# Kernel tuning notes

Hardware: AMD Instinct MI355X
Metric: run time of the kernel (lower is better)

The kernel has to match this reference:

```python
import jax, jax.numpy as jnp
import numpy as np

B, S, D, H = 2, 2048, 1024, 16
DH = D // H  # 64


def setup_inputs() -> dict:
    key = jax.random.key(0)
    k1, k2, k3, k4 = jax.random.split(key, 4)
    x = jax.random.normal(k1, (B, S, D), dtype=jnp.float32)
    # causal mask: 0 => masked (matches mask==0 -> -inf in source)
    mask = jnp.tril(jnp.ones((S, S), dtype=jnp.int32))
    Wq = jax.random.normal(k2, (H, D, DH), dtype=jnp.float32) * (D ** -0.5)
    Wk = jax.random.normal(k3, (H, D, DH), dtype=jnp.float32) * (D ** -0.5)
    Wo = jax.random.normal(k4, (D, D), dtype=jnp.float32) * (D ** -0.5)
    bo = jnp.zeros((D,), dtype=jnp.float32)
    return {"x": x, "mask": mask, "Wq": Wq, "Wk": Wk, "Wo": Wo, "bo": bo}


def reference(x, mask, Wq, Wk, Wo, bo):
    # Per source: q = query(x), k = key(x), v = query(x)  (bug kept: v == q)
    q = jnp.einsum('bsd,hde->bhse', x, Wq)   # [B,H,S,DH]
    k = jnp.einsum('bsd,hde->bhse', x, Wk)   # [B,H,S,DH]
    # scale uses d_model (input dim), not d_head -- faithful to source
    scale = jnp.asarray(D, x.dtype) ** -0.5
    scores = jnp.einsum('bhse,bhte->bhst', q, k) * scale  # [B,H,S,S]
    neg_inf = jnp.asarray(float('-inf'), scores.dtype)
    scores = jnp.where(mask[None, None, :, :] == 0, neg_inf, scores)
    w = jax.nn.softmax(scores, axis=-1)
    attn = jnp.einsum('bhst,bhte->bhse', w, q)  # v == q
    # concat heads: head axis becomes contiguous feature blocks
    attn = attn.transpose(0, 2, 1, 3).reshape(B, S, D)
    return attn @ Wo + bo
```

## Files before the change

kernel.cpp:

```cpp
#include <hip/hip_runtime.h>
#include <hip/hip_bf16.h>

#define BQ 2
#define SQ 2048
#define DMODEL 1024
#define NH 16
#define DH 64
#define NQT (SQ / 64)

typedef __attribute__((ext_vector_type(8))) short bf16x8;
typedef __attribute__((ext_vector_type(4))) short bf16x4;
typedef __attribute__((ext_vector_type(4))) float f32x4;
typedef unsigned short u16;

__device__ __forceinline__ u16 f2b(float f) {
  __hip_bfloat16 h = __float2bfloat16(f);
  return *reinterpret_cast<u16*>(&h);
}

__device__ __forceinline__ unsigned packbf(float lo, float hi) {
  return ((unsigned)f2b(hi) << 16) | (unsigned)f2b(lo);
}

#define MFMA(a, b, c) __builtin_amdgcn_mfma_f32_16x16x32_bf16((a), (b), (c), 0, 0, 0)

__device__ __forceinline__ f32x4 mfma16(bf16x4 a, bf16x4 b, f32x4 c) {
  asm("v_mfma_f32_16x16x16_bf16 %0, %1, %2, %0" : "+v"(c) : "v"(a), "v"(b));
  return c;
}

__device__ __forceinline__ unsigned cvtpk(float lo, float hi) {
  unsigned r;
  asm("v_cvt_pk_bf16_f32 %0, %1, %2" : "=v"(r) : "v"(lo), "v"(hi));
  return r;
}

#define CS (0.03125f * 1.44269504088896f)

__global__ __launch_bounds__(256) void prep_kernel(
    const float* __restrict__ Wq, const float* __restrict__ Wk,
    const float* __restrict__ Wo, const float* __restrict__ x,
    u16* __restrict__ WqT, u16* __restrict__ WkT, u16* __restrict__ WoT,
    u16* __restrict__ xb) {
  __shared__ alignas(16) u16 T[64][72];
  int xt = blockIdx.x, yt = blockIdx.y, z = blockIdx.z;
  int tid = threadIdx.x;
  if (z == 3) {
    int idx = (yt * 16 + xt) * 256 + tid;
    const int nchunks = BQ * SQ * DMODEL / 4;
    for (int i = idx; i < nchunks; i += 65536) {
      float4 v = *(const float4*)&x[(size_t)i * 4];
      uint2 o;
      o.x = packbf(v.x, v.y);
      o.y = packbf(v.z, v.w);
      *(uint2*)&xb[(size_t)i * 4] = o;
    }
    return;
  }
  if (z < 2) {
    const float* W = z ? Wk : Wq;
    u16* WT = z ? WkT : WqT;
    const float* src = W + ((size_t)yt * 1024 + xt * 64) * 64;
#pragma unroll
    for (int i = 0; i < 4; ++i) {
      int lin = tid + i * 256;
      int r = lin >> 4, c4 = (lin & 15) * 4;
      float4 v = *(const float4*)&src[(size_t)r * 64 + c4];
      *(unsigned*)&T[r][c4]     = packbf(v.x, v.y);
      *(unsigned*)&T[r][c4 + 2] = packbf(v.z, v.w);
    }
    __syncthreads();
#pragma unroll
    for (int i = 0; i < 2; ++i) {
      int lin = tid + i * 256;
      int e = lin >> 3, d8 = (lin & 7) * 8;
      u16 tmp[8];
#pragma unroll
      for (int j = 0; j < 8; ++j) tmp[j] = T[d8 + j][e];
      *(uint4*)&WT[((size_t)yt * 64 + e) * 1024 + xt * 64 + d8] = *(uint4*)tmp;
    }
  } else {
    const float* src = Wo + ((size_t)xt * 64) * 1024 + yt * 64;
#pragma unroll
    for (int i = 0; i < 4; ++i) {
      int lin = tid + i * 256;
      int r = lin >> 4, c4 = (lin & 15) * 4;
      float4 v = *(const float4*)&src[(size_t)r * 1024 + c4];
      *(unsigned*)&T[r][c4]     = packbf(v.x, v.y);
      *(unsigned*)&T[r][c4 + 2] = packbf(v.z, v.w);
    }
    __syncthreads();
#pragma unroll
    for (int i = 0; i < 2; ++i) {
      int lin = tid + i * 256;
      int n = lin >> 3, k8 = (lin & 7) * 8;
      u16 tmp[8];
#pragma unroll
      for (int j = 0; j < 8; ++j) tmp[j] = T[k8 + j][n];
      *(uint4*)&WoT[((size_t)yt * 64 + n) * 1024 + xt * 64 + k8] = *(uint4*)tmp;
    }
  }
}

__global__ __launch_bounds__(256) void transpose_q_kernel(
    const u16* __restrict__ Q, u16* __restrict__ QT) {
  __shared__ alignas(16) u16 T[64][72];
  int st = blockIdx.x, h = blockIdx.y, b = blockIdx.z;
  size_t hb = ((size_t)(b * NH + h)) * SQ * DH;
  int tid = threadIdx.x;
#pragma unroll
  for (int i2 = 0; i2 < 2; ++i2) {
    int c = tid + i2 * 256;
    int r = c >> 3, cc = (c & 7) * 8;
    *(uint4*)&T[r][cc] = *(const uint4*)&Q[hb + (size_t)(st * 64 + r) * DH + cc];
  }
  __syncthreads();
#pragma unroll
  for (int i2 = 0; i2 < 2; ++i2) {
    int c = tid + i2 * 256;
    int e = c >> 3, s8 = (c & 7) * 8;
    u16 tmp[8];
#pragma unroll
    for (int j = 0; j < 8; ++j) tmp[j] = T[s8 + j][e];
    *(uint4*)&QT[hb + (size_t)e * SQ + st * 64 + s8] = *(uint4*)tmp;
  }
}


__global__ __launch_bounds__(256) void proj_kernel(
    const u16* __restrict__ xb,
    const u16* __restrict__ Wcat,
    u16* __restrict__ Qb, u16* __restrict__ Kb,
    u16* __restrict__ QT) {
  __shared__ alignas(16) u16 Xs[64][72];
  __shared__ alignas(16) u16 Ws[64][72];
  int st = blockIdx.x, hy = blockIdx.y, b = blockIdx.z;
  int tid = threadIdx.x, w = tid >> 6, l = tid & 63;
  int lr = l & 15, hi = l >> 4, lk = hi * 8;
  int r0s = tid >> 3, cc0 = (tid & 7) * 8, r1s = r0s + 32;
  f32x4 acc[4] = {};
  const u16* Ab = xb + (size_t)(b * SQ + st * 64) * DMODEL;
  const u16* Wb = Wcat + (size_t)hy * DH * DMODEL;

  *(uint4*)&Xs[r0s][cc0] = *(const uint4*)&Ab[(size_t)r0s * DMODEL + cc0];
  *(uint4*)&Xs[r1s][cc0] = *(const uint4*)&Ab[(size_t)r1s * DMODEL + cc0];
  *(uint4*)&Ws[r0s][cc0] = *(const uint4*)&Wb[(size_t)r0s * DMODEL + cc0];
  *(uint4*)&Ws[r1s][cc0] = *(const uint4*)&Wb[(size_t)r1s * DMODEL + cc0];
  __syncthreads();

  uint4 xr0 = *(const uint4*)&Ab[(size_t)r0s * DMODEL + 64 + cc0];
  uint4 xr1 = *(const uint4*)&Ab[(size_t)r1s * DMODEL + 64 + cc0];
  uint4 wv0 = *(const uint4*)&Wb[(size_t)r0s * DMODEL + 64 + cc0];
  uint4 wv1 = *(const uint4*)&Wb[(size_t)r1s * DMODEL + 64 + cc0];

  for (int ks = 0; ks < 16; ++ks) {
#pragma unroll
    for (int kk = 0; kk < 2; ++kk) {
      bf16x8 a = *(const bf16x8*)&Xs[w * 16 + lr][kk * 32 + lk];
#pragma unroll
      for (int n = 0; n < 4; ++n) {
        bf16x8 bb = *(const bf16x8*)&Ws[n * 16 + lr][kk * 32 + lk];
        acc[n] = MFMA(a, bb, acc[n]);
      }
    }
    if (ks < 15) {
      __syncthreads();
      *(uint4*)&Xs[r0s][cc0] = xr0;
      *(uint4*)&Xs[r1s][cc0] = xr1;
      *(uint4*)&Ws[r0s][cc0] = wv0;
      *(uint4*)&Ws[r1s][cc0] = wv1;
      if (ks + 2 < 16) {
        int k0 = (ks + 2) * 64;
        xr0 = *(const uint4*)&Ab[(size_t)r0s * DMODEL + k0 + cc0];
        xr1 = *(const uint4*)&Ab[(size_t)r1s * DMODEL + k0 + cc0];
        wv0 = *(const uint4*)&Wb[(size_t)r0s * DMODEL + k0 + cc0];
        wv1 = *(const uint4*)&Wb[(size_t)r1s * DMODEL + k0 + cc0];
      }
      __syncthreads();
    }
  }

  bool isQ = (hy < NH);
  float scale = isQ ? 1.0f : CS;
  int hh = hy & (NH - 1);
  size_t hbh = ((size_t)(b * NH + hh)) * SQ * DH;
  size_t obase = hbh + (size_t)st * 64 * DH;
  int r0 = w * 16 + (hi << 2);
  u16 (*Cs)[72] = Xs;
  __syncthreads();
#pragma unroll
  for (int n = 0; n < 4; ++n)
#pragma unroll
    for (int r = 0; r < 4; ++r)
      Cs[r0 + r][n * 16 + lr] = f2b(acc[n][r] * scale);
  __syncthreads();

  u16* dst = isQ ? Qb : Kb;
#pragma unroll
  for (int i2 = 0; i2 < 2; ++i2) {
    int lin = tid + i2 * 256;
    int r = lin >> 3, c8 = (lin & 7) * 8;
    *(uint4*)&dst[obase + (size_t)r * DH + c8] = *(const uint4*)&Cs[r][c8];
  }
  if (isQ && QT) {
#pragma unroll
    for (int i2 = 0; i2 < 2; ++i2) {
      int lin = tid + i2 * 256;
      int e = lin >> 3, s8 = (lin & 7) * 8;
      u16 tmp[8];
#pragma unroll
      for (int j = 0; j < 8; ++j) tmp[j] = Cs[s8 + j][e];
      *(uint4*)&QT[hbh + (size_t)e * SQ + st * 64 + s8] = *(uint4*)tmp;
    }
  }
}


__global__ __launch_bounds__(512) void attn_kernel(
    const u16* __restrict__ Qt,
    const u16* __restrict__ Kt,
    const u16* __restrict__ QTt,
    u16* __restrict__ Oc) {
  __shared__ alignas(16) u16 Ks[2][64][72];
  __shared__ alignas(16) u16 Vs[2][64][72];
  int bx = blockIdx.x, h = blockIdx.y, b = blockIdx.z;
  int p = b ? bx : (15 - bx);
  int tid = threadIdx.x, w = tid >> 6, l = tid & 63;
  int lr = l & 15, hi = l >> 4, lk = hi * 8;
  int qtile = 2 * p + (w >> 2);
  int q0 = qtile * 64 + (w & 3) * 16;
  int jmax = 2 * p + 1;
  size_t hb = ((size_t)(b * NH + h)) * SQ * DH;

  int r0s = tid >> 3, cc0 = (tid & 7) * 8;

  bf16x8 aq[2];
  {
    const u16* qrow = Qt + hb + (size_t)(q0 + lr) * DH;
    aq[0] = *(const bf16x8*)&qrow[lk];
    aq[1] = *(const bf16x8*)&qrow[32 + lk];
  }

  *(uint4*)&Ks[0][r0s][cc0] = *(const uint4*)&Kt[hb + (size_t)r0s * DH + cc0];
  *(uint4*)&Vs[0][r0s][cc0] = *(const uint4*)&QTt[hb + (size_t)r0s * SQ + cc0];
  __syncthreads();

  uint4 kreg = *(const uint4*)&Kt[hb + (size_t)(64 + r0s) * DH + cc0];
  uint4 vreg = *(const uint4*)&QTt[hb + (size_t)r0s * SQ + 64 + cc0];

  f32x4 acc_t[4] = {};
  float l_run = 0.f;
  int cur = 0;

  for (int j = 0; j <= jmax; ++j) {
    if (j <= qtile) {
      f32x4 s[4] = {};
#pragma unroll
      for (int kk = 0; kk < 2; ++kk)
#pragma unroll
        for (int n = 0; n < 4; ++n) {
          bf16x8 bk = *(const bf16x8*)&Ks[cur][n * 16 + lr][kk * 32 + lk];
          s[n] = MFMA(bk, aq[kk], s[n]);
        }

      if (j == qtile) {
        int qg = q0 + lr;
#pragma unroll
        for (int n = 0; n < 4; ++n) {
          int kbase = j * 64 + n * 16 + hi * 4;
#pragma unroll
          for (int r = 0; r < 4; ++r)
            s[n][r] = (kbase + r > qg) ? 0.f : exp2f(s[n][r]);
        }
      } else {
#pragma unroll
        for (int n = 0; n < 4; ++n)
#pragma unroll
          for (int r = 0; r < 4; ++r) s[n][r] = exp2f(s[n][r]);
      }

#pragma unroll
      for (int n = 0; n < 4; ++n)
        l_run += (s[n][0] + s[n][1]) + (s[n][2] + s[n][3]);

      bf16x4 pb[4];
#pragma unroll
      for (int n = 0; n < 4; ++n) {
        uint2 u;
        u.x = cvtpk(s[n][0], s[n][1]);
        u.y = cvtpk(s[n][2], s[n][3]);
        pb[n] = *(bf16x4*)&u;
      }

#pragma unroll
      for (int nv = 0; nv < 4; ++nv) {
        const u16* vrow = &Vs[cur][nv * 16 + lr][hi * 4];
#pragma unroll
        for (int nh = 0; nh < 4; ++nh) {
          bf16x4 va = *(const bf16x4*)&vrow[nh * 16];
          acc_t[nv] = mfma16(va, pb[nh], acc_t[nv]);
        }
      }
    }

    if (j < jmax) {
      *(uint4*)&Ks[cur ^ 1][r0s][cc0] = kreg;
      *(uint4*)&Vs[cur ^ 1][r0s][cc0] = vreg;
      if (j + 2 <= jmax) {
        kreg = *(const uint4*)&Kt[hb + (size_t)((j + 2) * 64 + r0s) * DH + cc0];
        vreg = *(const uint4*)&QTt[hb + (size_t)r0s * SQ + (j + 2) * 64 + cc0];
      }
      __syncthreads();
      cur ^= 1;
    }
  }

  l_run += __shfl_xor(l_run, 16, 64);
  l_run += __shfl_xor(l_run, 32, 64);
  float inv = 1.f / l_run;

  size_t rbase = ((size_t)b * SQ + q0 + lr) * DMODEL + h * DH;
#pragma unroll
  for (int nv = 0; nv < 4; ++nv) {
    uint2 pw;
    pw.x = cvtpk(acc_t[nv][0] * inv, acc_t[nv][1] * inv);
    pw.y = cvtpk(acc_t[nv][2] * inv, acc_t[nv][3] * inv);
    *(uint2*)&Oc[rbase + nv * 16 + hi * 4] = pw;
  }
}


__global__ __launch_bounds__(256) void outproj_kernel(
    const u16* __restrict__ Oc,
    const u16* __restrict__ WoT,
    const float* __restrict__ bo,
    float* __restrict__ out) {
  __shared__ alignas(16) u16 Xs[64][72];
  __shared__ alignas(16) u16 Ws[64][72];
  int rt = blockIdx.x, nt = blockIdx.y;
  int tid = threadIdx.x, w = tid >> 6, l = tid & 63;
  int lr = l & 15, lk = (l >> 4) * 8;
  int r0s = tid >> 3, cc0 = (tid & 7) * 8, r1s = r0s + 32;
  f32x4 acc[4] = {};
  const u16* Ab = Oc + (size_t)rt * 64 * DMODEL;
  const u16* Wb = WoT + (size_t)nt * 64 * DMODEL;

  *(uint4*)&Xs[r0s][cc0] = *(const uint4*)&Ab[(size_t)r0s * DMODEL + cc0];
  *(uint4*)&Xs[r1s][cc0] = *(const uint4*)&Ab[(size_t)r1s * DMODEL + cc0];
  *(uint4*)&Ws[r0s][cc0] = *(const uint4*)&Wb[(size_t)r0s * DMODEL + cc0];
  *(uint4*)&Ws[r1s][cc0] = *(const uint4*)&Wb[(size_t)r1s * DMODEL + cc0];
  __syncthreads();

  uint4 xr0 = *(const uint4*)&Ab[(size_t)r0s * DMODEL + 64 + cc0];
  uint4 xr1 = *(const uint4*)&Ab[(size_t)r1s * DMODEL + 64 + cc0];
  uint4 wv0 = *(const uint4*)&Wb[(size_t)r0s * DMODEL + 64 + cc0];
  uint4 wv1 = *(const uint4*)&Wb[(size_t)r1s * DMODEL + 64 + cc0];

  for (int ks = 0; ks < 16; ++ks) {
#pragma unroll
    for (int kk = 0; kk < 2; ++kk) {
      bf16x8 a = *(const bf16x8*)&Xs[w * 16 + lr][kk * 32 + lk];
#pragma unroll
      for (int n = 0; n < 4; ++n) {
        bf16x8 bb = *(const bf16x8*)&Ws[n * 16 + lr][kk * 32 + lk];
        acc[n] = MFMA(a, bb, acc[n]);
      }
    }
    if (ks < 15) {
      __syncthreads();
      *(uint4*)&Xs[r0s][cc0] = xr0;
      *(uint4*)&Xs[r1s][cc0] = xr1;
      *(uint4*)&Ws[r0s][cc0] = wv0;
      *(uint4*)&Ws[r1s][cc0] = wv1;
      if (ks + 2 < 16) {
        int k0 = (ks + 2) * 64;
        xr0 = *(const uint4*)&Ab[(size_t)r0s * DMODEL + k0 + cc0];
        xr1 = *(const uint4*)&Ab[(size_t)r1s * DMODEL + k0 + cc0];
        wv0 = *(const uint4*)&Wb[(size_t)r0s * DMODEL + k0 + cc0];
        wv1 = *(const uint4*)&Wb[(size_t)r1s * DMODEL + k0 + cc0];
      }
      __syncthreads();
    }
  }

  int r0 = w * 16 + ((l >> 4) << 2);
#pragma unroll
  for (int n = 0; n < 4; ++n) {
    int col = nt * 64 + n * 16 + lr;
    float bv = bo[col];
#pragma unroll
    for (int r = 0; r < 4; ++r)
      out[(size_t)(rt * 64 + r0 + r) * DMODEL + col] = acc[n][r] + bv;
  }
}


extern "C" void kernel_launch(void* const* d_in, const int* in_sizes, int n_in,
                              void* d_out, int out_size, void* d_ws, size_t ws_size,
                              hipStream_t stream) {
  const float* x  = (const float*)d_in[0];
  const float* Wq = (const float*)d_in[2];
  const float* Wk = (const float*)d_in[3];
  const float* Wo = (const float*)d_in[4];
  const float* bo = (const float*)d_in[5];
  float* out = (float*)d_out;

  char* ws = (char*)d_ws;
  u16* xb  = (u16*)ws;
  u16* WqT = xb + (size_t)BQ * SQ * DMODEL;
  u16* WkT = WqT + (size_t)NH * DH * DMODEL;
  u16* WoT = WkT + (size_t)NH * DH * DMODEL;
  u16* Qb  = WoT + (size_t)DMODEL * DMODEL;
  u16* Kb  = Qb + (size_t)BQ * NH * SQ * DH;
  u16* Ob  = Kb + (size_t)BQ * NH * SQ * DH;
  u16* QTnew = Ob + (size_t)BQ * SQ * DMODEL;

  size_t need = ((size_t)QTnew - (size_t)ws) + (size_t)BQ * SQ * DMODEL * sizeof(u16);
  bool fused = ws_size >= need;
  u16* QTb = fused ? QTnew : xb;

  prep_kernel<<<dim3(16, 16, 4), 256, 0, stream>>>(Wq, Wk, Wo, x, WqT, WkT, WoT, xb);

  proj_kernel<<<dim3(SQ / 64, 2 * NH, BQ), 256, 0, stream>>>(
      xb, WqT, Qb, Kb, fused ? QTb : (u16*)nullptr);
  if (!fused)
    transpose_q_kernel<<<dim3(SQ / 64, NH, BQ), 256, 0, stream>>>(Qb, QTb);
  attn_kernel<<<dim3(16, NH, BQ), 512, 0, stream>>>(Qb, Kb, QTb, Ob);
  outproj_kernel<<<dim3(BQ * SQ / 64, DMODEL / 64, 1), 256, 0, stream>>>(Ob, WoT, bo, out);
}
```

Baseline: 107.3 us.

## Split KV range across two wave groups per query tile and reduce partials

The attention kernel previously gave each block a pair of query tiles (paired for causal load balance), with both 4-wave groups sharing a serial double-buffered KV loop. Now each block handles one query tile, and the two wave groups process alternating KV tiles (even/odd) in parallel. Their partial accumulators and row sums are combined through shared memory at the end. The grid doubles to 32 query tiles per head, giving more blocks and shorter per-block serial chains. In exchange it adds an extra sync per iteration, a reduction step, and uneven block durations under the causal mask.

```diff
diff --git a/kernel.cpp b/kernel.cpp
--- a/kernel.cpp
+++ b/kernel.cpp
@@ -224,14 +224,12 @@
   __shared__ alignas(16) u16 Ks[2][64][72];
   __shared__ alignas(16) u16 Vs[2][64][72];
   int bx = blockIdx.x, h = blockIdx.y, b = blockIdx.z;
-  int p = b ? bx : (15 - bx);
   int tid = threadIdx.x, w = tid >> 6, l = tid & 63;
   int lr = l & 15, hi = l >> 4, lk = hi * 8;
-  int qtile = 2 * p + (w >> 2);
-  int q0 = qtile * 64 + (w & 3) * 16;
-  int jmax = 2 * p + 1;
+  int g = w >> 2, wb = w & 3;
+  int qtile = NQT - 1 - bx;
+  int q0 = qtile * 64 + wb * 16;
   size_t hb = ((size_t)(b * NH + h)) * SQ * DH;
-
   int r0s = tid >> 3, cc0 = (tid & 7) * 8;
 
   bf16x8 aq[2];
@@ -243,31 +241,45 @@
 
   *(uint4*)&Ks[0][r0s][cc0] = *(const uint4*)&Kt[hb + (size_t)r0s * DH + cc0];
   *(uint4*)&Vs[0][r0s][cc0] = *(const uint4*)&QTt[hb + (size_t)r0s * SQ + cc0];
-  __syncthreads();
-
-  uint4 kreg = *(const uint4*)&Kt[hb + (size_t)(64 + r0s) * DH + cc0];
-  uint4 vreg = *(const uint4*)&QTt[hb + (size_t)r0s * SQ + 64 + cc0];
+  if (qtile >= 1) {
+    *(uint4*)&Ks[1][r0s][cc0] = *(const uint4*)&Kt[hb + (size_t)(64 + r0s) * DH + cc0];
+    *(uint4*)&Vs[1][r0s][cc0] = *(const uint4*)&QTt[hb + (size_t)r0s * SQ + 64 + cc0];
+  }
+  __syncthreads();
 
   f32x4 acc_t[4] = {};
   float l_run = 0.f;
-  int cur = 0;
-
-  for (int j = 0; j <= jmax; ++j) {
-    if (j <= qtile) {
+  int niter = (qtile >> 1) + 1;
+
+  for (int i = 0; i < niter; ++i) {
+    uint4 k0r, v0r, k1r, v1r;
+    int t0n = 2 * i + 2, t1n = 2 * i + 3;
+    bool h0 = (t0n <= qtile), h1 = (t1n <= qtile);
+    if (h0) {
+      k0r = *(const uint4*)&Kt[hb + (size_t)(t0n * 64 + r0s) * DH + cc0];
+      v0r = *(const uint4*)&QTt[hb + (size_t)r0s * SQ + t0n * 64 + cc0];
+    }
+    if (h1) {
+      k1r = *(const uint4*)&Kt[hb + (size_t)(t1n * 64 + r0s) * DH + cc0];
+      v1r = *(const uint4*)&QTt[hb + (size_t)r0s * SQ + t1n * 64 + cc0];
+    }
+
+    int t = 2 * i + g;
+    if (t <= qtile) {
       f32x4 s[4] = {};
 #pragma unroll
       for (int kk = 0; kk < 2; ++kk)
 #pragma unroll
         for (int n = 0; n < 4; ++n) {
-          bf16x8 bk = *(const bf16x8*)&Ks[cur][n * 16 + lr][kk * 32 + lk];
+          bf16x8 bk = *(const bf16x8*)&Ks[g][n * 16 + lr][kk * 32 + lk];
           s[n] = MFMA(bk, aq[kk], s[n]);
         }
 
-      if (j == qtile) {
+      if (t == qtile) {
         int qg = q0 + lr;
 #pragma unroll
         for (int n = 0; n < 4; ++n) {
-          int kbase = j * 64 + n * 16 + hi * 4;
+          int kbase = t * 64 + n * 16 + hi * 4;
 #pragma unroll
           for (int r = 0; r < 4; ++r)
             s[n][r] = (kbase + r > qg) ? 0.f : exp2f(s[n][r]);
@@ -294,7 +306,7 @@
 
 #pragma unroll
       for (int nv = 0; nv < 4; ++nv) {
-        const u16* vrow = &Vs[cur][nv * 16 + lr][hi * 4];
+        const u16* vrow = &Vs[g][nv * 16 + lr][hi * 4];
 #pragma unroll
         for (int nh = 0; nh < 4; ++nh) {
           bf16x4 va = *(const bf16x4*)&vrow[nh * 16];
@@ -303,29 +315,43 @@
       }
     }
 
-    if (j < jmax) {
-      *(uint4*)&Ks[cur ^ 1][r0s][cc0] = kreg;
-      *(uint4*)&Vs[cur ^ 1][r0s][cc0] = vreg;
-      if (j + 2 <= jmax) {
-        kreg = *(const uint4*)&Kt[hb + (size_t)((j + 2) * 64 + r0s) * DH + cc0];
-        vreg = *(const uint4*)&QTt[hb + (size_t)r0s * SQ + (j + 2) * 64 + cc0];
-      }
-      __syncthreads();
-      cur ^= 1;
-    }
-  }
-
-  l_run += __shfl_xor(l_run, 16, 64);
-  l_run += __shfl_xor(l_run, 32, 64);
-  float inv = 1.f / l_run;
-
-  size_t rbase = ((size_t)b * SQ + q0 + lr) * DMODEL + h * DH;
-#pragma unroll
-  for (int nv = 0; nv < 4; ++nv) {
-    uint2 pw;
-    pw.x = cvtpk(acc_t[nv][0] * inv, acc_t[nv][1] * inv);
-    pw.y = cvtpk(acc_t[nv][2] * inv, acc_t[nv][3] * inv);
-    *(uint2*)&Oc[rbase + nv * 16 + hi * 4] = pw;
+    if (i + 1 < niter) {
+      __syncthreads();
+      if (h0) { *(uint4*)&Ks[0][r0s][cc0] = k0r; *(uint4*)&Vs[0][r0s][cc0] = v0r; }
+      if (h1) { *(uint4*)&Ks[1][r0s][cc0] = k1r; *(uint4*)&Vs[1][r0s][cc0] = v1r; }
+      __syncthreads();
+    }
+  }
+
+  __syncthreads();
+  float* red = (float*)&Ks[0][0][0];
+  int base = (wb * 64 + l) * 17;
+  if (g == 1) {
+#pragma unroll
+    for (int nv = 0; nv < 4; ++nv)
+#pragma unroll
+      for (int r = 0; r < 4; ++r) red[base + nv * 4 + r] = acc_t[nv][r];
+    red[base + 16] = l_run;
+  }
+  __syncthreads();
+  if (g == 0) {
+#pragma unroll
+    for (int nv = 0; nv < 4; ++nv)
+#pragma unroll
+      for (int r = 0; r < 4; ++r) acc_t[nv][r] += red[base + nv * 4 + r];
+    l_run += red[base + 16];
+
+    l_run += __shfl_xor(l_run, 16, 64);
+    l_run += __shfl_xor(l_run, 32, 64);
+    float inv = 1.f / l_run;
+    size_t rbase = ((size_t)b * SQ + q0 + lr) * DMODEL + h * DH;
+#pragma unroll
+    for (int nv = 0; nv < 4; ++nv) {
+      uint2 pw;
+      pw.x = cvtpk(acc_t[nv][0] * inv, acc_t[nv][1] * inv);
+      pw.y = cvtpk(acc_t[nv][2] * inv, acc_t[nv][3] * inv);
+      *(uint2*)&Oc[rbase + nv * 16 + hi * 4] = pw;
+    }
   }
 }
 
@@ -425,6 +451,6 @@
       xb, WqT, Qb, Kb, fused ? QTb : (u16*)nullptr);
   if (!fused)
     transpose_q_kernel<<<dim3(SQ / 64, NH, BQ), 256, 0, stream>>>(Qb, QTb);
-  attn_kernel<<<dim3(16, NH, BQ), 512, 0, stream>>>(Qb, Kb, QTb, Ob);
+  attn_kernel<<<dim3(NQT, NH, BQ), 512, 0, stream>>>(Qb, Kb, QTb, Ob);
   outproj_kernel<<<dim3(BQ * SQ / 64, DMODEL / 64, 1), 256, 0, stream>>>(Ob, WoT, bo, out);
 }
```

New measurement: 139.9 us. 30.4% more time.
